# Kernel tuning notes

Hardware: AMD Instinct MI355X
Metric: run time of the kernel (lower is better)

Reference implementation:

```python
import jax, jax.numpy as jnp
import numpy as np

B, H, W, C = 4, 64, 64, 32
M1 = M2 = 16
N = H * W          # 4096 grid nodes per sample
E = 131072         # edges (avg degree 32)
EDIM = 6           # edge feature dim
KMID = 64          # kernel MLP hidden width
EPS = 1e-5         # InstanceNorm eps


def _gelu(x):
    return jax.nn.gelu(x, approximate=False)  # torch nn.GELU default is exact erf


def _mlp(x, w1, b1, w2, b2):
    return _gelu(x @ w1 + b1) @ w2 + b2


def _inorm(x):
    # torch InstanceNorm2d(affine=False) applied to [B,H,W,C]: normalizes over last two dims
    m = x.mean(axis=(2, 3), keepdims=True)
    v = x.var(axis=(2, 3), keepdims=True)
    return (x - m) * jax.lax.rsqrt(v + EPS)


def _lin_init(k, fin, fout):
    lim = 1.0 / np.sqrt(fin)
    kw, kb = jax.random.split(k)
    w = jax.random.uniform(kw, (fin, fout), jnp.float32, -lim, lim)
    b = jax.random.uniform(kb, (fout,), jnp.float32, -lim, lim)
    return w, b


def setup_inputs() -> dict:
    key = jax.random.key(0)
    ks = jax.random.split(key, 14)
    s = 1.0 / (C * C)
    inp = {}
    inp['nodes'] = jax.random.normal(ks[0], (B, H, W, C), jnp.float32)
    inp['edge_index'] = jax.random.randint(ks[1], (2, E), 0, N, dtype=jnp.int64)
    inp['edge_attr'] = jax.random.uniform(ks[2], (E, EDIM), jnp.float32)
    # spectral conv complex weights, stored as real/imag float32 pairs
    inp['w1_re'] = s * jax.random.uniform(ks[3], (C, C, M1, M2), jnp.float32)
    inp['w1_im'] = s * jax.random.uniform(ks[4], (C, C, M1, M2), jnp.float32)
    inp['w2_re'] = s * jax.random.uniform(ks[5], (C, C, M1, M2), jnp.float32)
    inp['w2_im'] = s * jax.random.uniform(ks[6], (C, C, M1, M2), jnp.float32)
    # self.mlp : MLP(C, C, 2C)
    inp['mlp_w1'], inp['mlp_b1'] = _lin_init(ks[7], C, 2 * C)
    inp['mlp_w2'], inp['mlp_b2'] = _lin_init(ks[8], 2 * C, C)
    # self.w : MLP(C, C, 2C)
    inp['wm_w1'], inp['wm_b1'] = _lin_init(ks[9], C, 2 * C)
    inp['wm_w2'], inp['wm_b2'] = _lin_init(ks[10], 2 * C, C)
    # GNO kernel MLP : EDIM -> KMID -> C*C
    inp['ker_w1'], inp['ker_b1'] = _lin_init(ks[11], EDIM, KMID)
    inp['ker_w2'], inp['ker_b2'] = _lin_init(ks[12], KMID, C * C)
    # NNConv root weight and bias (PyG uniform(size) init with size=in_channels)
    lim = 1.0 / np.sqrt(C)
    kr, kb = jax.random.split(ks[13])
    inp['root'] = jax.random.uniform(kr, (C, C), jnp.float32, -lim, lim)
    inp['gbias'] = jax.random.uniform(kb, (C,), jnp.float32, -lim, lim)
    return inp


def reference(nodes, edge_index, edge_attr, w1_re, w1_im, w2_re, w2_im,
              mlp_w1, mlp_b1, mlp_w2, mlp_b2, wm_w1, wm_b1, wm_w2, wm_b2,
              ker_w1, ker_b1, ker_w2, ker_b2, root, gbias):
    x = _inorm(nodes)                                             # [B,H,W,C]

    # --- spectral conv branch ---
    x_ft = jnp.fft.rfftn(x, axes=(1, 2), norm='ortho')            # [B,H,W//2+1,C]
    w1 = (w1_re + 1j * w1_im).astype(jnp.complex64)
    w2 = (w2_re + 1j * w2_im).astype(jnp.complex64)
    top = jnp.einsum('bxyi,ioxy->bxyo', x_ft[:, :M1, :M2, :], w1)
    bot = jnp.einsum('bxyi,ioxy->bxyo', x_ft[:, -M1:, :M2, :], w2)
    out_ft = jnp.zeros((B, H, W // 2 + 1, C), jnp.complex64)
    out_ft = out_ft.at[:, :M1, :M2, :].set(top).at[:, -M1:, :M2, :].set(bot)
    x1 = jnp.fft.irfftn(out_ft, axes=(1, 2), s=(H, W), norm='ortho')
    x1 = _mlp(_inorm(x1), mlp_w1, mlp_b1, mlp_w2, mlp_b2)         # [B,H,W,C]

    # --- pointwise MLP branch ---
    x2 = _inorm(_mlp(x, wm_w1, wm_b1, wm_w2, wm_b2))              # [B,H,W,C]

    # --- edge-conditioned GNO branch ---
    x3 = x.reshape(B, N, C)
    wmat = _mlp(edge_attr, ker_w1, ker_b1, ker_w2, ker_b2).reshape(E, C, C)
    src, dst = edge_index[0], edge_index[1]
    msg = jnp.einsum('bec,eco->beo', x3[:, src, :], wmat)         # [B,E,C]
    agg = jnp.zeros((B, N, C), jnp.float32).at[:, dst, :].add(msg)
    x3 = agg + x3 @ root + gbias                                  # [B,N,C]

    return _gelu(x1 + x2 + x3.reshape(B, H, W, C))
```

## Files before the change

### kernel.cpp

```cpp
#include <hip/hip_runtime.h>

#define B_ 4
#define H_ 64
#define W_ 64
#define C_ 32
#define N_ 4096
#define E_ 131072

typedef _Float16 half8 __attribute__((ext_vector_type(8)));
typedef float f32x4 __attribute__((ext_vector_type(4)));

__device__ __forceinline__ float gelu_f(float x) {
    return 0.5f * x * (1.0f + erff(x * 0.70710678118654752f));
}

#define TWOPI_64 (6.2831853071795864769f / 64.0f)

__device__ __forceinline__ void block_reduce2(float& s, float& s2, float* red) {
    #pragma unroll
    for (int off = 32; off > 0; off >>= 1) {
        s  += __shfl_down(s, off, 64);
        s2 += __shfl_down(s2, off, 64);
    }
    int lane = threadIdx.x & 63, wv = threadIdx.x >> 6;
    __syncthreads();
    if (lane == 0) { red[wv] = s; red[wv + 4] = s2; }
    __syncthreads();
    s  = red[0] + red[1] + red[2] + red[3];
    s2 = red[4] + red[5] + red[6] + red[7];
}

__global__ __launch_bounds__(256, 4) void k_pre(const float* __restrict__ nodes,
                                                const float* __restrict__ w2,
                                                float* __restrict__ xn,
                                                float* __restrict__ agg,
                                                float* __restrict__ Gre, float* __restrict__ Gim,
                                                _Float16* __restrict__ whi, _Float16* __restrict__ wlo) {
    int t = threadIdx.x;
    if (blockIdx.x >= 256) {
        int g0 = (blockIdx.x - 256) * 512 + t;
        #pragma unroll 1
        for (int rep = 0; rep < 2; ++rep) {
            int g = g0 + rep * 256;
            int j = g & 7, l = (g >> 3) & 63, fid = g >> 9;
            int i = fid >> 2, t2 = (fid >> 1) & 1, kh = fid & 1;
            int quad = l >> 4, l15 = l & 15;
            int k = kh * 32 + quad * 8 + j;
            int n = i * 32 + t2 * 16 + l15;
            float v = w2[k * 1024 + n];
            _Float16 hi = (_Float16)v;
            whi[g] = hi;
            wlo[g] = (_Float16)(v - (float)hi);
        }
        return;
    }
    int bh = blockIdx.x;
    __shared__ float sx[2048];
    __shared__ float tc[64], ts[64];
    __shared__ float red[8];
    const float4* src = (const float4*)(nodes + bh * 2048);
    float4* dst = (float4*)(xn + bh * 2048);
    float4* az = (float4*)(agg + bh * 2048);
    if (t < 64) { float a = TWOPI_64 * t; tc[t] = cosf(a); ts[t] = sinf(a); }
    float4 v0 = src[t * 2], v1 = src[t * 2 + 1];
    float s  = v0.x + v0.y + v0.z + v0.w + v1.x + v1.y + v1.z + v1.w;
    float s2 = v0.x*v0.x + v0.y*v0.y + v0.z*v0.z + v0.w*v0.w
             + v1.x*v1.x + v1.y*v1.y + v1.z*v1.z + v1.w*v1.w;
    block_reduce2(s, s2, red);
    float mean = s * (1.0f / 2048.0f);
    float var  = s2 * (1.0f / 2048.0f) - mean * mean;
    float sc = rsqrtf(var + 1e-5f);
    v0.x = (v0.x - mean) * sc; v0.y = (v0.y - mean) * sc;
    v0.z = (v0.z - mean) * sc; v0.w = (v0.w - mean) * sc;
    v1.x = (v1.x - mean) * sc; v1.y = (v1.y - mean) * sc;
    v1.z = (v1.z - mean) * sc; v1.w = (v1.w - mean) * sc;
    dst[t * 2] = v0; dst[t * 2 + 1] = v1;
    float4 z = {0.f, 0.f, 0.f, 0.f};
    az[t * 2] = z; az[t * 2 + 1] = z;
    ((float4*)sx)[t * 2] = v0;
    ((float4*)sx)[t * 2 + 1] = v1;
    __syncthreads();
    #pragma unroll 1
    for (int rep = 0; rep < 2; ++rep) {
        int oi = rep * 256 + t;
        int ky = oi >> 5, i = oi & 31;
        float re = 0.f, im = 0.f;
        #pragma unroll 8
        for (int w = 0; w < 64; ++w) {
            float v = sx[w * 32 + i];
            int m = (ky * w) & 63;
            re += v * tc[m];
            im -= v * ts[m];
        }
        Gre[bh * 512 + oi] = re;
        Gim[bh * 512 + oi] = im;
    }
}

__global__ __launch_bounds__(256, 4) void k_gnofxy(
        const float* __restrict__ Gre, const float* __restrict__ Gim,
        const float* __restrict__ w1re, const float* __restrict__ w1im,
        const float* __restrict__ w2re, const float* __restrict__ w2im,
        float* __restrict__ Yr, float* __restrict__ Yi,
        const float* __restrict__ ea,
        const float* __restrict__ kw1, const float* __restrict__ kb1,
        const float* __restrict__ kb2,
        const _Float16* __restrict__ whi, const _Float16* __restrict__ wlo,
        const float* __restrict__ xn,
        const int* __restrict__ ei,
        float* __restrict__ agg) {
    __shared__ __align__(16) float sbufF[4624];
    __shared__ float sB2[1024];
    __shared__ int ssrc[64], sdst[64];
    int t = threadIdx.x;

    if (blockIdx.x < 128) {
        float* tc  = sbufF;
        float* ts  = sbufF + 64;
        float* sXr = sbufF + 128;
        float* sXi = sbufF + 656;
        int bid = blockIdx.x;
        int b = bid >> 5, kxi = bid & 31;
        int kx = kxi + (kxi < 16 ? 0 : 32);
        int x = kxi & 15;
        const float* wre = (kxi < 16) ? w1re : w2re;
        const float* wim = (kxi < 16) ? w1im : w2im;
        if (t < 64) { float a = TWOPI_64 * t; tc[t] = cosf(a); ts[t] = sinf(a); }
        __syncthreads();
        #pragma unroll 1
        for (int rep = 0; rep < 2; ++rep) {
            int oi = rep * 256 + t;
            int ky = oi >> 5, i = oi & 31;
            float re = 0.f, im = 0.f;
            #pragma unroll 8
            for (int h = 0; h < 64; ++h) {
                int gidx = (b * 64 + h) * 512 + ky * 32 + i;
                float gr = Gre[gidx], gi = Gim[gidx];
                int m = (kx * h) & 63;
                float c = tc[m], sv = ts[m];
                re += gr * c + gi * sv;
                im += gi * c - gr * sv;
            }
            sXr[ky * 33 + i] = re;
            sXi[ky * 33 + i] = im;
        }
        __syncthreads();
        #pragma unroll 1
        for (int rep = 0; rep < 2; ++rep) {
            int oi = rep * 256 + t;
            int ky = oi & 15, o = oi >> 4;
            float re = 0.f, im = 0.f;
            #pragma unroll 4
            for (int i = 0; i < 32; ++i) {
                float xr = sXr[ky * 33 + i], xi = sXi[ky * 33 + i];
                int widx = (i * 32 + o) * 256 + x * 16 + ky;
                float wr = wre[widx], wi = wim[widx];
                re += xr * wr - xi * wi;
                im += xr * wi + xi * wr;
            }
            Yr[bid * 512 + ky * 32 + o] = re;
            Yi[bid * 512 + ky * 32 + o] = im;
        }
        return;
    }

    _Float16* sxTh = (_Float16*)sbufF;
    int lane = t & 63, wv = t >> 6, quad = lane >> 4, l15 = lane & 15;
    int eg = wv >> 1;
    int t2 = wv & 1;
    int e0 = (blockIdx.x - 128) * 64;

    if (t < 64) ssrc[t] = ei[e0 + t];
    else if (t < 128) sdst[t - 64] = ei[E_ + e0 + t - 64];
    for (int f = t; f < 1024; f += 256) sB2[f] = kb2[f];
    {
        int r = t >> 2, k0 = (t & 3) * 16;
        const float* ep = ea + (e0 + r) * 6;
        float e6[6];
        #pragma unroll
        for (int d = 0; d < 6; ++d) e6[d] = ep[d];
        #pragma unroll
        for (int kk = 0; kk < 16; ++kk) {
            int k = k0 + kk;
            float acc = kb1[k];
            #pragma unroll
            for (int d = 0; d < 6; ++d) acc += e6[d] * kw1[d * 64 + k];
            sbufF[r * 68 + k] = gelu_f(acc);
        }
    }
    __syncthreads();

    half8 ahi[2][2], alo[2][2];
    #pragma unroll
    for (int et = 0; et < 2; ++et) {
        #pragma unroll
        for (int kh = 0; kh < 2; ++kh) {
            const float* hp = sbufF + (eg * 32 + et * 16 + l15) * 68 + kh * 32 + quad * 8;
            float4 h0 = *(const float4*)hp;
            float4 h1 = *(const float4*)(hp + 4);
            float hv[8] = {h0.x, h0.y, h0.z, h0.w, h1.x, h1.y, h1.z, h1.w};
            half8 hh, hl;
            #pragma unroll
            for (int j = 0; j < 8; ++j) {
                _Float16 hi = (_Float16)hv[j];
                hh[j] = hi;
                hl[j] = (_Float16)(hv[j] - (float)hi);
            }
            ahi[et][kh] = hh;
            alo[et][kh] = hl;
        }
    }
    __syncthreads();

    {
        int b = t & 3, r = t >> 2;
        int s = ssrc[r];
        int pe = (r >> 5) * 32 + ((r >> 2) & 3) * 8 + ((r >> 4) & 1) * 4 + (r & 3);
        const float4* xp = (const float4*)(xn + (b * 4096 + s) * 32);
        _Float16* dp = sxTh + b * 2312 + pe;
        #pragma unroll
        for (int q = 0; q < 8; ++q) {
            float4 v = xp[q];
            dp[(q * 4 + 0) * 72] = (_Float16)v.x;
            dp[(q * 4 + 1) * 72] = (_Float16)v.y;
            dp[(q * 4 + 2) * 72] = (_Float16)v.z;
            dp[(q * 4 + 3) * 72] = (_Float16)v.w;
        }
    }
    __syncthreads();

    float msg[4][2][4];
    #pragma unroll
    for (int b = 0; b < 4; ++b)
        #pragma unroll
        for (int et = 0; et < 2; ++et)
            #pragma unroll
            for (int r = 0; r < 4; ++r) msg[b][et][r] = 0.f;

    for (int i = 0; i < 32; ++i) {
        float b2v = sB2[i * 32 + t2 * 16 + l15];
        int f0 = (i * 4 + t2 * 2) * 512 + lane * 8;
        half8 bhi0 = *(const half8*)(whi + f0);
        half8 bhi1 = *(const half8*)(whi + f0 + 512);
        half8 blo0 = *(const half8*)(wlo + f0);
        half8 blo1 = *(const half8*)(wlo + f0 + 512);
        f32x4 acc[2];
        #pragma unroll
        for (int et = 0; et < 2; ++et) {
            f32x4 a = {b2v, b2v, b2v, b2v};
            a = __builtin_amdgcn_mfma_f32_16x16x32_f16(ahi[et][0], bhi0, a, 0, 0, 0);
            a = __builtin_amdgcn_mfma_f32_16x16x32_f16(ahi[et][1], bhi1, a, 0, 0, 0);
            a = __builtin_amdgcn_mfma_f32_16x16x32_f16(ahi[et][0], blo0, a, 0, 0, 0);
            a = __builtin_amdgcn_mfma_f32_16x16x32_f16(ahi[et][1], blo1, a, 0, 0, 0);
            a = __builtin_amdgcn_mfma_f32_16x16x32_f16(alo[et][0], bhi0, a, 0, 0, 0);
            a = __builtin_amdgcn_mfma_f32_16x16x32_f16(alo[et][1], bhi1, a, 0, 0, 0);
            acc[et] = a;
        }
        #pragma unroll
        for (int b = 0; b < 4; ++b) {
            const half8 xv = *(const half8*)(sxTh + b * 2312 + i * 72 + eg * 32 + quad * 8);
            #pragma unroll
            for (int et = 0; et < 2; ++et) {
                msg[b][et][0] += (float)xv[et * 4 + 0] * acc[et][0];
                msg[b][et][1] += (float)xv[et * 4 + 1] * acc[et][1];
                msg[b][et][2] += (float)xv[et * 4 + 2] * acc[et][2];
                msg[b][et][3] += (float)xv[et * 4 + 3] * acc[et][3];
            }
        }
    }

    int o = t2 * 16 + l15;
    #pragma unroll
    for (int et = 0; et < 2; ++et) {
        #pragma unroll
        for (int r = 0; r < 4; ++r) {
            int row = eg * 32 + et * 16 + quad * 4 + r;
            int d = sdst[row];
            #pragma unroll
            for (int b = 0; b < 4; ++b) {
                atomicAdd(&agg[(b * 4096 + d) * 32 + o], msg[b][et][r]);
            }
        }
    }
}

__global__ __launch_bounds__(256, 4) void k_zx12(const float* __restrict__ Yr, const float* __restrict__ Yi,
                                                 const float* __restrict__ mw1, const float* __restrict__ mb1,
                                                 const float* __restrict__ mw2, const float* __restrict__ mb2,
                                                 const float* __restrict__ ww1, const float* __restrict__ wb1,
                                                 const float* __restrict__ ww2, const float* __restrict__ wb2,
                                                 const float* __restrict__ xn,
                                                 float* __restrict__ osum) {
    int bh = blockIdx.x;
    int b = bh >> 6, h = bh & 63;
    int t = threadIdx.x;
    __shared__ float tc[64], ts[64];
    __shared__ float red[8];
    __shared__ float sZr[528], sZi[528];
    __shared__ float sP[2112];
    __shared__ float sH[4160];
    __shared__ float sW1[2048], sW2[2048];
    __shared__ float sX[2112];
    if (t < 64) { float a = TWOPI_64 * t; tc[t] = cosf(a); ts[t] = sinf(a); }
    for (int f = t; f < 2048; f += 256) { sW1[f] = mw1[f]; sW2[f] = mw2[f]; }
    __syncthreads();
    #pragma unroll 1
    for (int rep = 0; rep < 2; ++rep) {
        int oi = rep * 256 + t;
        int ky = oi >> 5, o = oi & 31;
        float re = 0.f, im = 0.f;
        #pragma unroll 4
        for (int kxi = 0; kxi < 32; ++kxi) {
            int kx = kxi + (kxi < 16 ? 0 : 32);
            int m = (kx * h) & 63;
            float c = tc[m], sv = ts[m];
            int yidx = (b * 32 + kxi) * 512 + ky * 32 + o;
            float yr = Yr[yidx], yi = Yi[yidx];
            re += yr * c - yi * sv;
            im += yr * sv + yi * c;
        }
        sZr[ky * 33 + o] = re;
        sZi[ky * 33 + o] = im;
    }
    __syncthreads();
    float s = 0.f, s2 = 0.f;
    #pragma unroll 1
    for (int rep = 0; rep < 8; ++rep) {
        int idx = rep * 256 + t;
        int w = idx >> 5, o = idx & 31;
        float acc = sZr[o];
        #pragma unroll
        for (int ky = 1; ky < 16; ++ky) {
            int m = (ky * w) & 63;
            acc += 2.0f * (sZr[ky * 33 + o] * tc[m] - sZi[ky * 33 + o] * ts[m]);
        }
        acc *= (1.0f / 4096.0f);
        sP[w * 33 + o] = acc;
        s += acc; s2 += acc * acc;
    }
    block_reduce2(s, s2, red);
    float mean = s * (1.0f / 2048.0f);
    float sc = rsqrtf(s2 * (1.0f / 2048.0f) - mean * mean + 1e-5f);
    #pragma unroll 1
    for (int rep = 0; rep < 8; ++rep) {
        int idx = rep * 256 + t;
        int w = idx >> 5, o = idx & 31;
        sP[w * 33 + o] = (sP[w * 33 + o] - mean) * sc;
    }
    __syncthreads();
    #pragma unroll 1
    for (int rep = 0; rep < 16; ++rep) {
        int idx = rep * 256 + t;
        int w = idx >> 6, k = idx & 63;
        float acc = mb1[k];
        #pragma unroll 4
        for (int c = 0; c < 32; ++c) acc += sP[w * 33 + c] * sW1[c * 64 + k];
        sH[w * 65 + k] = gelu_f(acc);
    }
    __syncthreads();
    #pragma unroll 1
    for (int rep = 0; rep < 8; ++rep) {
        int idx = rep * 256 + t;
        int w = idx >> 5, o = idx & 31;
        float acc = mb2[o];
        #pragma unroll 4
        for (int k = 0; k < 64; ++k) acc += sH[w * 65 + k] * sW2[k * 32 + o];
        sP[w * 33 + o] = acc;
        sX[w * 33 + o] = xn[bh * 2048 + idx];
    }
    __syncthreads();
    for (int f = t; f < 2048; f += 256) { sW1[f] = ww1[f]; sW2[f] = ww2[f]; }
    __syncthreads();
    #pragma unroll 1
    for (int rep = 0; rep < 16; ++rep) {
        int idx = rep * 256 + t;
        int w = idx >> 6, k = idx & 63;
        float acc = wb1[k];
        #pragma unroll 4
        for (int c = 0; c < 32; ++c) acc += sX[w * 33 + c] * sW1[c * 64 + k];
        sH[w * 65 + k] = gelu_f(acc);
    }
    __syncthreads();
    s = 0.f; s2 = 0.f;
    #pragma unroll 1
    for (int rep = 0; rep < 8; ++rep) {
        int idx = rep * 256 + t;
        int w = idx >> 5, o = idx & 31;
        float acc = wb2[o];
        #pragma unroll 4
        for (int k = 0; k < 64; ++k) acc += sH[w * 65 + k] * sW2[k * 32 + o];
        sX[w * 33 + o] = acc;
        s += acc; s2 += acc * acc;
    }
    block_reduce2(s, s2, red);
    mean = s * (1.0f / 2048.0f);
    sc = rsqrtf(s2 * (1.0f / 2048.0f) - mean * mean + 1e-5f);
    #pragma unroll 1
    for (int rep = 0; rep < 8; ++rep) {
        int idx = rep * 256 + t;
        int w = idx >> 5, o = idx & 31;
        osum[bh * 2048 + idx] = sP[w * 33 + o] + (sX[w * 33 + o] - mean) * sc;
    }
}

__global__ __launch_bounds__(256, 4) void k_final(const float* __restrict__ osum, const float* __restrict__ agg,
                                                  const float* __restrict__ xn, const float* __restrict__ root,
                                                  const float* __restrict__ gbias, float* __restrict__ out) {
    int bh = blockIdx.x;
    int t = threadIdx.x;
    __shared__ float sX[64 * 33];
    __shared__ float sR[1024];
    for (int f = t; f < 2048; f += 256) sX[(f >> 5) * 33 + (f & 31)] = xn[bh * 2048 + f];
    for (int f = t; f < 1024; f += 256) sR[f] = root[f];
    __syncthreads();
    #pragma unroll 1
    for (int rep = 0; rep < 8; ++rep) {
        int idx = rep * 256 + t;
        int w = idx >> 5, o = idx & 31;
        float acc = gbias[o] + osum[bh * 2048 + idx] + agg[bh * 2048 + idx];
        #pragma unroll 4
        for (int c = 0; c < 32; ++c) acc += sX[w * 33 + c] * sR[c * 32 + o];
        out[bh * 2048 + idx] = gelu_f(acc);
    }
}

extern "C" void kernel_launch(void* const* d_in, const int* in_sizes, int n_in,
                              void* d_out, int out_size, void* d_ws, size_t ws_size,
                              hipStream_t stream) {
    (void)in_sizes; (void)n_in; (void)out_size; (void)ws_size;
    const float* nodes  = (const float*)d_in[0];
    const int*   eidx   = (const int*)d_in[1];
    const float* eattr  = (const float*)d_in[2];
    const float* w1re   = (const float*)d_in[3];
    const float* w1im   = (const float*)d_in[4];
    const float* w2re   = (const float*)d_in[5];
    const float* w2im   = (const float*)d_in[6];
    const float* mlp_w1 = (const float*)d_in[7];
    const float* mlp_b1 = (const float*)d_in[8];
    const float* mlp_w2 = (const float*)d_in[9];
    const float* mlp_b2 = (const float*)d_in[10];
    const float* wm_w1  = (const float*)d_in[11];
    const float* wm_b1  = (const float*)d_in[12];
    const float* wm_w2  = (const float*)d_in[13];
    const float* wm_b2  = (const float*)d_in[14];
    const float* ker_w1 = (const float*)d_in[15];
    const float* ker_b1 = (const float*)d_in[16];
    const float* ker_w2 = (const float*)d_in[17];
    const float* ker_b2 = (const float*)d_in[18];
    const float* root   = (const float*)d_in[19];
    const float* gbias  = (const float*)d_in[20];
    float* out = (float*)d_out;

    char* ws = (char*)d_ws;
    size_t off = 0;
    auto alloc = [&](size_t bytes) {
        void* p = ws + off;
        off += (bytes + 255) & ~(size_t)255;
        return p;
    };
    float* xn   = (float*)alloc(524288 * 4);
    float* agg  = (float*)alloc(524288 * 4);
    float* osum = (float*)alloc(524288 * 4);
    float* Gre  = (float*)alloc(131072 * 4);
    float* Gim  = (float*)alloc(131072 * 4);
    float* Yr   = (float*)alloc(65536 * 4);
    float* Yi   = (float*)alloc(65536 * 4);
    _Float16* whi = (_Float16*)alloc(65536 * 2);
    _Float16* wlo = (_Float16*)alloc(65536 * 2);

    k_pre<<<384, 256, 0, stream>>>(nodes, ker_w2, xn, agg, Gre, Gim, whi, wlo);
    k_gnofxy<<<2176, 256, 0, stream>>>(Gre, Gim, w1re, w1im, w2re, w2im, Yr, Yi,
                                       eattr, ker_w1, ker_b1, ker_b2, whi, wlo, xn, eidx, agg);
    k_zx12<<<256, 256, 0, stream>>>(Yr, Yi, mlp_w1, mlp_b1, mlp_w2, mlp_b2,
                                    wm_w1, wm_b1, wm_w2, wm_b2, xn, osum);
    k_final<<<256, 256, 0, stream>>>(osum, agg, xn, root, gbias, out);
}
```

Baseline: 254.0 us.

## Split GNO edge blocks across two kernels to overlap spectral stages

Factors the edge-message GNO work into a shared device function and splits its 2048 edge blocks: 1408 run alongside the forward spectral contraction in k_g1, and the remaining 640 run alongside the inverse DFT plus the spectral MLP in k_g2. The pointwise MLP branch with its InstanceNorm moves into the final kernel, which also fuses the root matmul and GELU. The aim is to fill idle compute units during the small spectral stages with independent GNO work. The cost is larger shared-memory footprints, which may lower occupancy, and a heavier final kernel running at lower launch-bounds occupancy.

```diff
diff --git a/kernel.cpp b/kernel.cpp
--- a/kernel.cpp
+++ b/kernel.cpp
@@ -1,10 +1,5 @@
 #include <hip/hip_runtime.h>
 
-#define B_ 4
-#define H_ 64
-#define W_ 64
-#define C_ 32
-#define N_ 4096
 #define E_ 131072
 
 typedef _Float16 half8 __attribute__((ext_vector_type(8)));
@@ -28,6 +23,128 @@
     __syncthreads();
     s  = red[0] + red[1] + red[2] + red[3];
     s2 = red[4] + red[5] + red[6] + red[7];
+}
+
+__device__ __forceinline__ void gno_body(int e0, float* sbufF, float* sB2, int* ssrc, int* sdst,
+                                         const float* __restrict__ ea,
+                                         const float* __restrict__ kw1, const float* __restrict__ kb1,
+                                         const float* __restrict__ kb2,
+                                         const _Float16* __restrict__ whi, const _Float16* __restrict__ wlo,
+                                         const float* __restrict__ xn, const int* __restrict__ ei,
+                                         float* __restrict__ agg) {
+    _Float16* sxTh = (_Float16*)sbufF;
+    int t = threadIdx.x;
+    int lane = t & 63, wv = t >> 6, quad = lane >> 4, l15 = lane & 15;
+    int eg = wv >> 1, t2 = wv & 1;
+
+    if (t < 64) ssrc[t] = ei[e0 + t];
+    else if (t < 128) sdst[t - 64] = ei[E_ + e0 + t - 64];
+    for (int f = t; f < 1024; f += 256) sB2[f] = kb2[f];
+    {
+        int r = t >> 2, k0 = (t & 3) * 16;
+        const float* ep = ea + (e0 + r) * 6;
+        float e6[6];
+        #pragma unroll
+        for (int d = 0; d < 6; ++d) e6[d] = ep[d];
+        #pragma unroll
+        for (int kk = 0; kk < 16; ++kk) {
+            int k = k0 + kk;
+            float acc = kb1[k];
+            #pragma unroll
+            for (int d = 0; d < 6; ++d) acc += e6[d] * kw1[d * 64 + k];
+            sbufF[r * 68 + k] = gelu_f(acc);
+        }
+    }
+    __syncthreads();
+    half8 ahi[2][2], alo[2][2];
+    #pragma unroll
+    for (int et = 0; et < 2; ++et) {
+        #pragma unroll
+        for (int kh = 0; kh < 2; ++kh) {
+            const float* hp = sbufF + (eg * 32 + et * 16 + l15) * 68 + kh * 32 + quad * 8;
+            float4 h0 = *(const float4*)hp;
+            float4 h1 = *(const float4*)(hp + 4);
+            float hv[8] = {h0.x, h0.y, h0.z, h0.w, h1.x, h1.y, h1.z, h1.w};
+            half8 hh, hl;
+            #pragma unroll
+            for (int j = 0; j < 8; ++j) {
+                _Float16 hi = (_Float16)hv[j];
+                hh[j] = hi;
+                hl[j] = (_Float16)(hv[j] - (float)hi);
+            }
+            ahi[et][kh] = hh;
+            alo[et][kh] = hl;
+        }
+    }
+    __syncthreads();
+    {
+        int b = t & 3, r = t >> 2;
+        int s = ssrc[r];
+        int pe = (r >> 5) * 32 + ((r >> 2) & 3) * 8 + ((r >> 4) & 1) * 4 + (r & 3);
+        const float4* xp = (const float4*)(xn + (b * 4096 + s) * 32);
+        _Float16* dp = sxTh + b * 2312 + pe;
+        #pragma unroll
+        for (int q = 0; q < 8; ++q) {
+            float4 v = xp[q];
+            dp[(q * 4 + 0) * 72] = (_Float16)v.x;
+            dp[(q * 4 + 1) * 72] = (_Float16)v.y;
+            dp[(q * 4 + 2) * 72] = (_Float16)v.z;
+            dp[(q * 4 + 3) * 72] = (_Float16)v.w;
+        }
+    }
+    __syncthreads();
+    float msg[4][2][4];
+    #pragma unroll
+    for (int b = 0; b < 4; ++b)
+        #pragma unroll
+        for (int et = 0; et < 2; ++et)
+            #pragma unroll
+            for (int r = 0; r < 4; ++r) msg[b][et][r] = 0.f;
+
+    for (int i = 0; i < 32; ++i) {
+        float b2v = sB2[i * 32 + t2 * 16 + l15];
+        int f0 = (i * 4 + t2 * 2) * 512 + lane * 8;
+        half8 bhi0 = *(const half8*)(whi + f0);
+        half8 bhi1 = *(const half8*)(whi + f0 + 512);
+        half8 blo0 = *(const half8*)(wlo + f0);
+        half8 blo1 = *(const half8*)(wlo + f0 + 512);
+        f32x4 acc[2];
+        #pragma unroll
+        for (int et = 0; et < 2; ++et) {
+            f32x4 ac = {b2v, b2v, b2v, b2v};
+            ac = __builtin_amdgcn_mfma_f32_16x16x32_f16(ahi[et][0], bhi0, ac, 0, 0, 0);
+            ac = __builtin_amdgcn_mfma_f32_16x16x32_f16(ahi[et][1], bhi1, ac, 0, 0, 0);
+            ac = __builtin_amdgcn_mfma_f32_16x16x32_f16(ahi[et][0], blo0, ac, 0, 0, 0);
+            ac = __builtin_amdgcn_mfma_f32_16x16x32_f16(ahi[et][1], blo1, ac, 0, 0, 0);
+            ac = __builtin_amdgcn_mfma_f32_16x16x32_f16(alo[et][0], bhi0, ac, 0, 0, 0);
+            ac = __builtin_amdgcn_mfma_f32_16x16x32_f16(alo[et][1], bhi1, ac, 0, 0, 0);
+            acc[et] = ac;
+        }
+        #pragma unroll
+        for (int b = 0; b < 4; ++b) {
+            const half8 xv = *(const half8*)(sxTh + b * 2312 + i * 72 + eg * 32 + quad * 8);
+            #pragma unroll
+            for (int et = 0; et < 2; ++et) {
+                msg[b][et][0] += (float)xv[et * 4 + 0] * acc[et][0];
+                msg[b][et][1] += (float)xv[et * 4 + 1] * acc[et][1];
+                msg[b][et][2] += (float)xv[et * 4 + 2] * acc[et][2];
+                msg[b][et][3] += (float)xv[et * 4 + 3] * acc[et][3];
+            }
+        }
+    }
+    int o = t2 * 16 + l15;
+    #pragma unroll
+    for (int et = 0; et < 2; ++et) {
+        #pragma unroll
+        for (int r = 0; r < 4; ++r) {
+            int row = eg * 32 + et * 16 + quad * 4 + r;
+            int d = sdst[row];
+            #pragma unroll
+            for (int b = 0; b < 4; ++b) {
+                atomicAdd(&agg[(b * 4096 + d) * 32 + o], msg[b][et][r]);
+            }
+        }
+    }
 }
 
 __global__ __launch_bounds__(256, 4) void k_pre(const float* __restrict__ nodes,
@@ -97,7 +214,7 @@
     }
 }
 
-__global__ __launch_bounds__(256, 4) void k_gnofxy(
+__global__ __launch_bounds__(256, 4) void k_g1(
         const float* __restrict__ Gre, const float* __restrict__ Gim,
         const float* __restrict__ w1re, const float* __restrict__ w1im,
         const float* __restrict__ w2re, const float* __restrict__ w2im,
@@ -109,16 +226,15 @@
         const float* __restrict__ xn,
         const int* __restrict__ ei,
         float* __restrict__ agg) {
-    __shared__ __align__(16) float sbufF[4624];
-    __shared__ float sB2[1024];
+    __shared__ __align__(16) float U[5648];
     __shared__ int ssrc[64], sdst[64];
     int t = threadIdx.x;
 
     if (blockIdx.x < 128) {
-        float* tc  = sbufF;
-        float* ts  = sbufF + 64;
-        float* sXr = sbufF + 128;
-        float* sXi = sbufF + 656;
+        float* tc  = U;
+        float* ts  = U + 64;
+        float* sXr = U + 128;
+        float* sXi = U + 656;
         int bid = blockIdx.x;
         int b = bid >> 5, kxi = bid & 31;
         int kx = kxi + (kxi < 16 ? 0 : 32);
@@ -163,213 +279,129 @@
         }
         return;
     }
-
-    _Float16* sxTh = (_Float16*)sbufF;
-    int lane = t & 63, wv = t >> 6, quad = lane >> 4, l15 = lane & 15;
-    int eg = wv >> 1;
-    int t2 = wv & 1;
-    int e0 = (blockIdx.x - 128) * 64;
-
-    if (t < 64) ssrc[t] = ei[e0 + t];
-    else if (t < 128) sdst[t - 64] = ei[E_ + e0 + t - 64];
-    for (int f = t; f < 1024; f += 256) sB2[f] = kb2[f];
-    {
-        int r = t >> 2, k0 = (t & 3) * 16;
-        const float* ep = ea + (e0 + r) * 6;
-        float e6[6];
-        #pragma unroll
-        for (int d = 0; d < 6; ++d) e6[d] = ep[d];
-        #pragma unroll
-        for (int kk = 0; kk < 16; ++kk) {
-            int k = k0 + kk;
-            float acc = kb1[k];
-            #pragma unroll
-            for (int d = 0; d < 6; ++d) acc += e6[d] * kw1[d * 64 + k];
-            sbufF[r * 68 + k] = gelu_f(acc);
-        }
-    }
-    __syncthreads();
-
-    half8 ahi[2][2], alo[2][2];
-    #pragma unroll
-    for (int et = 0; et < 2; ++et) {
-        #pragma unroll
-        for (int kh = 0; kh < 2; ++kh) {
-            const float* hp = sbufF + (eg * 32 + et * 16 + l15) * 68 + kh * 32 + quad * 8;
-            float4 h0 = *(const float4*)hp;
-            float4 h1 = *(const float4*)(hp + 4);
-            float hv[8] = {h0.x, h0.y, h0.z, h0.w, h1.x, h1.y, h1.z, h1.w};
-            half8 hh, hl;
-            #pragma unroll
-            for (int j = 0; j < 8; ++j) {
-                _Float16 hi = (_Float16)hv[j];
-                hh[j] = hi;
-                hl[j] = (_Float16)(hv[j] - (float)hi);
-            }
-            ahi[et][kh] = hh;
-            alo[et][kh] = hl;
-        }
-    }
-    __syncthreads();
-
-    {
-        int b = t & 3, r = t >> 2;
-        int s = ssrc[r];
-        int pe = (r >> 5) * 32 + ((r >> 2) & 3) * 8 + ((r >> 4) & 1) * 4 + (r & 3);
-        const float4* xp = (const float4*)(xn + (b * 4096 + s) * 32);
-        _Float16* dp = sxTh + b * 2312 + pe;
-        #pragma unroll
-        for (int q = 0; q < 8; ++q) {
-            float4 v = xp[q];
-            dp[(q * 4 + 0) * 72] = (_Float16)v.x;
-            dp[(q * 4 + 1) * 72] = (_Float16)v.y;
-            dp[(q * 4 + 2) * 72] = (_Float16)v.z;
-            dp[(q * 4 + 3) * 72] = (_Float16)v.w;
-        }
-    }
-    __syncthreads();
-
-    float msg[4][2][4];
-    #pragma unroll
-    for (int b = 0; b < 4; ++b)
-        #pragma unroll
-        for (int et = 0; et < 2; ++et)
-            #pragma unroll
-            for (int r = 0; r < 4; ++r) msg[b][et][r] = 0.f;
-
-    for (int i = 0; i < 32; ++i) {
-        float b2v = sB2[i * 32 + t2 * 16 + l15];
-        int f0 = (i * 4 + t2 * 2) * 512 + lane * 8;
-        half8 bhi0 = *(const half8*)(whi + f0);
-        half8 bhi1 = *(const half8*)(whi + f0 + 512);
-        half8 blo0 = *(const half8*)(wlo + f0);
-        half8 blo1 = *(const half8*)(wlo + f0 + 512);
-        f32x4 acc[2];
-        #pragma unroll
-        for (int et = 0; et < 2; ++et) {
-            f32x4 a = {b2v, b2v, b2v, b2v};
-            a = __builtin_amdgcn_mfma_f32_16x16x32_f16(ahi[et][0], bhi0, a, 0, 0, 0);
-            a = __builtin_amdgcn_mfma_f32_16x16x32_f16(ahi[et][1], bhi1, a, 0, 0, 0);
-            a = __builtin_amdgcn_mfma_f32_16x16x32_f16(ahi[et][0], blo0, a, 0, 0, 0);
-            a = __builtin_amdgcn_mfma_f32_16x16x32_f16(ahi[et][1], blo1, a, 0, 0, 0);
-            a = __builtin_amdgcn_mfma_f32_16x16x32_f16(alo[et][0], bhi0, a, 0, 0, 0);
-            a = __builtin_amdgcn_mfma_f32_16x16x32_f16(alo[et][1], bhi1, a, 0, 0, 0);
-            acc[et] = a;
-        }
-        #pragma unroll
-        for (int b = 0; b < 4; ++b) {
-            const half8 xv = *(const half8*)(sxTh + b * 2312 + i * 72 + eg * 32 + quad * 8);
-            #pragma unroll
-            for (int et = 0; et < 2; ++et) {
-                msg[b][et][0] += (float)xv[et * 4 + 0] * acc[et][0];
-                msg[b][et][1] += (float)xv[et * 4 + 1] * acc[et][1];
-                msg[b][et][2] += (float)xv[et * 4 + 2] * acc[et][2];
-                msg[b][et][3] += (float)xv[et * 4 + 3] * acc[et][3];
-            }
-        }
-    }
-
-    int o = t2 * 16 + l15;
-    #pragma unroll
-    for (int et = 0; et < 2; ++et) {
-        #pragma unroll
-        for (int r = 0; r < 4; ++r) {
-            int row = eg * 32 + et * 16 + quad * 4 + r;
-            int d = sdst[row];
-            #pragma unroll
-            for (int b = 0; b < 4; ++b) {
-                atomicAdd(&agg[(b * 4096 + d) * 32 + o], msg[b][et][r]);
-            }
-        }
-    }
-}
-
-__global__ __launch_bounds__(256, 4) void k_zx12(const float* __restrict__ Yr, const float* __restrict__ Yi,
-                                                 const float* __restrict__ mw1, const float* __restrict__ mb1,
-                                                 const float* __restrict__ mw2, const float* __restrict__ mb2,
-                                                 const float* __restrict__ ww1, const float* __restrict__ wb1,
-                                                 const float* __restrict__ ww2, const float* __restrict__ wb2,
-                                                 const float* __restrict__ xn,
-                                                 float* __restrict__ osum) {
+    gno_body((blockIdx.x - 128) * 64, U, U + 4624, ssrc, sdst,
+             ea, kw1, kb1, kb2, whi, wlo, xn, ei, agg);
+}
+
+__global__ __launch_bounds__(256, 4) void k_g2(
+        const float* __restrict__ Yr, const float* __restrict__ Yi,
+        const float* __restrict__ mw1, const float* __restrict__ mb1,
+        const float* __restrict__ mw2, const float* __restrict__ mb2,
+        float* __restrict__ osum,
+        const float* __restrict__ ea,
+        const float* __restrict__ kw1, const float* __restrict__ kb1,
+        const float* __restrict__ kb2,
+        const _Float16* __restrict__ whi, const _Float16* __restrict__ wlo,
+        const float* __restrict__ xn,
+        const int* __restrict__ ei,
+        float* __restrict__ agg) {
+    __shared__ __align__(16) float U[11584];
+    __shared__ int ssrc[64], sdst[64];
+    int t = threadIdx.x;
+
+    if (blockIdx.x < 256) {
+        int bh = blockIdx.x;
+        int b = bh >> 6, h = bh & 63;
+        float* tc  = U;
+        float* ts  = U + 64;
+        float* red = U + 128;
+        float* sZr = U + 136;
+        float* sZi = U + 664;
+        float* sP  = U + 1192;
+        float* sW1 = U + 3304;
+        float* sW2 = U + 5352;
+        float* sH  = U + 7400;
+        if (t < 64) { float a = TWOPI_64 * t; tc[t] = cosf(a); ts[t] = sinf(a); }
+        for (int f = t; f < 2048; f += 256) { sW1[f] = mw1[f]; sW2[f] = mw2[f]; }
+        __syncthreads();
+        #pragma unroll 1
+        for (int rep = 0; rep < 2; ++rep) {
+            int oi = rep * 256 + t;
+            int ky = oi >> 5, o = oi & 31;
+            float re = 0.f, im = 0.f;
+            #pragma unroll 4
+            for (int kxi = 0; kxi < 32; ++kxi) {
+                int kx = kxi + (kxi < 16 ? 0 : 32);
+                int m = (kx * h) & 63;
+                float c = tc[m], sv = ts[m];
+                int yidx = (b * 32 + kxi) * 512 + ky * 32 + o;
+                float yr = Yr[yidx], yi = Yi[yidx];
+                re += yr * c - yi * sv;
+                im += yr * sv + yi * c;
+            }
+            sZr[ky * 33 + o] = re;
+            sZi[ky * 33 + o] = im;
+        }
+        __syncthreads();
+        float s = 0.f, s2 = 0.f;
+        #pragma unroll 1
+        for (int rep = 0; rep < 8; ++rep) {
+            int idx = rep * 256 + t;
+            int w = idx >> 5, o = idx & 31;
+            float acc = sZr[o];
+            #pragma unroll
+            for (int ky = 1; ky < 16; ++ky) {
+                int m = (ky * w) & 63;
+                acc += 2.0f * (sZr[ky * 33 + o] * tc[m] - sZi[ky * 33 + o] * ts[m]);
+            }
+            acc *= (1.0f / 4096.0f);
+            sP[w * 33 + o] = acc;
+            s += acc; s2 += acc * acc;
+        }
+        block_reduce2(s, s2, red);
+        float mean = s * (1.0f / 2048.0f);
+        float sc = rsqrtf(s2 * (1.0f / 2048.0f) - mean * mean + 1e-5f);
+        #pragma unroll 1
+        for (int rep = 0; rep < 8; ++rep) {
+            int idx = rep * 256 + t;
+            int w = idx >> 5, o = idx & 31;
+            sP[w * 33 + o] = (sP[w * 33 + o] - mean) * sc;
+        }
+        __syncthreads();
+        #pragma unroll 1
+        for (int rep = 0; rep < 16; ++rep) {
+            int idx = rep * 256 + t;
+            int w = idx >> 6, k = idx & 63;
+            float acc = mb1[k];
+            #pragma unroll 4
+            for (int c = 0; c < 32; ++c) acc += sP[w * 33 + c] * sW1[c * 64 + k];
+            sH[w * 65 + k] = gelu_f(acc);
+        }
+        __syncthreads();
+        #pragma unroll 1
+        for (int rep = 0; rep < 8; ++rep) {
+            int idx = rep * 256 + t;
+            int w = idx >> 5, o = idx & 31;
+            float acc = mb2[o];
+            #pragma unroll 4
+            for (int k = 0; k < 64; ++k) acc += sH[w * 65 + k] * sW2[k * 32 + o];
+            osum[bh * 2048 + idx] = acc;
+        }
+        return;
+    }
+    gno_body((1408 + blockIdx.x - 256) * 64, U, U + 4624, ssrc, sdst,
+             ea, kw1, kb1, kb2, whi, wlo, xn, ei, agg);
+}
+
+__global__ __launch_bounds__(256, 2) void k_final2(const float* __restrict__ osum, const float* __restrict__ agg,
+                                                   const float* __restrict__ xn,
+                                                   const float* __restrict__ ww1, const float* __restrict__ wb1,
+                                                   const float* __restrict__ ww2, const float* __restrict__ wb2,
+                                                   const float* __restrict__ root, const float* __restrict__ gbias,
+                                                   float* __restrict__ out) {
     int bh = blockIdx.x;
-    int b = bh >> 6, h = bh & 63;
     int t = threadIdx.x;
-    __shared__ float tc[64], ts[64];
     __shared__ float red[8];
-    __shared__ float sZr[528], sZi[528];
-    __shared__ float sP[2112];
+    __shared__ float sX[2112];
     __shared__ float sH[4160];
     __shared__ float sW1[2048], sW2[2048];
-    __shared__ float sX[2112];
-    if (t < 64) { float a = TWOPI_64 * t; tc[t] = cosf(a); ts[t] = sinf(a); }
-    for (int f = t; f < 2048; f += 256) { sW1[f] = mw1[f]; sW2[f] = mw2[f]; }
-    __syncthreads();
-    #pragma unroll 1
-    for (int rep = 0; rep < 2; ++rep) {
-        int oi = rep * 256 + t;
-        int ky = oi >> 5, o = oi & 31;
-        float re = 0.f, im = 0.f;
-        #pragma unroll 4
-        for (int kxi = 0; kxi < 32; ++kxi) {
-            int kx = kxi + (kxi < 16 ? 0 : 32);
-            int m = (kx * h) & 63;
-            float c = tc[m], sv = ts[m];
-            int yidx = (b * 32 + kxi) * 512 + ky * 32 + o;
-            float yr = Yr[yidx], yi = Yi[yidx];
-            re += yr * c - yi * sv;
-            im += yr * sv + yi * c;
-        }
-        sZr[ky * 33 + o] = re;
-        sZi[ky * 33 + o] = im;
-    }
-    __syncthreads();
-    float s = 0.f, s2 = 0.f;
-    #pragma unroll 1
-    for (int rep = 0; rep < 8; ++rep) {
-        int idx = rep * 256 + t;
-        int w = idx >> 5, o = idx & 31;
-        float acc = sZr[o];
-        #pragma unroll
-        for (int ky = 1; ky < 16; ++ky) {
-            int m = (ky * w) & 63;
-            acc += 2.0f * (sZr[ky * 33 + o] * tc[m] - sZi[ky * 33 + o] * ts[m]);
-        }
-        acc *= (1.0f / 4096.0f);
-        sP[w * 33 + o] = acc;
-        s += acc; s2 += acc * acc;
-    }
-    block_reduce2(s, s2, red);
-    float mean = s * (1.0f / 2048.0f);
-    float sc = rsqrtf(s2 * (1.0f / 2048.0f) - mean * mean + 1e-5f);
-    #pragma unroll 1
-    for (int rep = 0; rep < 8; ++rep) {
-        int idx = rep * 256 + t;
-        int w = idx >> 5, o = idx & 31;
-        sP[w * 33 + o] = (sP[w * 33 + o] - mean) * sc;
-    }
-    __syncthreads();
-    #pragma unroll 1
-    for (int rep = 0; rep < 16; ++rep) {
-        int idx = rep * 256 + t;
-        int w = idx >> 6, k = idx & 63;
-        float acc = mb1[k];
-        #pragma unroll 4
-        for (int c = 0; c < 32; ++c) acc += sP[w * 33 + c] * sW1[c * 64 + k];
-        sH[w * 65 + k] = gelu_f(acc);
-    }
-    __syncthreads();
-    #pragma unroll 1
-    for (int rep = 0; rep < 8; ++rep) {
-        int idx = rep * 256 + t;
-        int w = idx >> 5, o = idx & 31;
-        float acc = mb2[o];
-        #pragma unroll 4
-        for (int k = 0; k < 64; ++k) acc += sH[w * 65 + k] * sW2[k * 32 + o];
-        sP[w * 33 + o] = acc;
-        sX[w * 33 + o] = xn[bh * 2048 + idx];
-    }
-    __syncthreads();
-    for (int f = t; f < 2048; f += 256) { sW1[f] = ww1[f]; sW2[f] = ww2[f]; }
+    __shared__ float sR[1024];
+    __shared__ float sP[2112];
+    for (int f = t; f < 2048; f += 256) {
+        sW1[f] = ww1[f]; sW2[f] = ww2[f];
+        sX[(f >> 5) * 33 + (f & 31)] = xn[bh * 2048 + f];
+    }
+    for (int f = t; f < 1024; f += 256) sR[f] = root[f];
     __syncthreads();
     #pragma unroll 1
     for (int rep = 0; rep < 16; ++rep) {
@@ -381,7 +413,7 @@
         sH[w * 65 + k] = gelu_f(acc);
     }
     __syncthreads();
-    s = 0.f; s2 = 0.f;
+    float s = 0.f, s2 = 0.f;
     #pragma unroll 1
     for (int rep = 0; rep < 8; ++rep) {
         int idx = rep * 256 + t;
@@ -389,35 +421,18 @@
         float acc = wb2[o];
         #pragma unroll 4
         for (int k = 0; k < 64; ++k) acc += sH[w * 65 + k] * sW2[k * 32 + o];
-        sX[w * 33 + o] = acc;
+        sP[w * 33 + o] = acc;
         s += acc; s2 += acc * acc;
     }
     block_reduce2(s, s2, red);
-    mean = s * (1.0f / 2048.0f);
-    sc = rsqrtf(s2 * (1.0f / 2048.0f) - mean * mean + 1e-5f);
+    float mean = s * (1.0f / 2048.0f);
+    float sc = rsqrtf(s2 * (1.0f / 2048.0f) - mean * mean + 1e-5f);
     #pragma unroll 1
     for (int rep = 0; rep < 8; ++rep) {
         int idx = rep * 256 + t;
         int w = idx >> 5, o = idx & 31;
-        osum[bh * 2048 + idx] = sP[w * 33 + o] + (sX[w * 33 + o] - mean) * sc;
-    }
-}
-
-__global__ __launch_bounds__(256, 4) void k_final(const float* __restrict__ osum, const float* __restrict__ agg,
-                                                  const float* __restrict__ xn, const float* __restrict__ root,
-                                                  const float* __restrict__ gbias, float* __restrict__ out) {
-    int bh = blockIdx.x;
-    int t = threadIdx.x;
-    __shared__ float sX[64 * 33];
-    __shared__ float sR[1024];
-    for (int f = t; f < 2048; f += 256) sX[(f >> 5) * 33 + (f & 31)] = xn[bh * 2048 + f];
-    for (int f = t; f < 1024; f += 256) sR[f] = root[f];
-    __syncthreads();
-    #pragma unroll 1
-    for (int rep = 0; rep < 8; ++rep) {
-        int idx = rep * 256 + t;
-        int w = idx >> 5, o = idx & 31;
-        float acc = gbias[o] + osum[bh * 2048 + idx] + agg[bh * 2048 + idx];
+        float acc = gbias[o] + osum[bh * 2048 + idx] + agg[bh * 2048 + idx]
+                  + (sP[w * 33 + o] - mean) * sc;
         #pragma unroll 4
         for (int c = 0; c < 32; ++c) acc += sX[w * 33 + c] * sR[c * 32 + o];
         out[bh * 2048 + idx] = gelu_f(acc);
@@ -469,9 +484,9 @@
     _Float16* wlo = (_Float16*)alloc(65536 * 2);
 
     k_pre<<<384, 256, 0, stream>>>(nodes, ker_w2, xn, agg, Gre, Gim, whi, wlo);
-    k_gnofxy<<<2176, 256, 0, stream>>>(Gre, Gim, w1re, w1im, w2re, w2im, Yr, Yi,
-                                       eattr, ker_w1, ker_b1, ker_b2, whi, wlo, xn, eidx, agg);
-    k_zx12<<<256, 256, 0, stream>>>(Yr, Yi, mlp_w1, mlp_b1, mlp_w2, mlp_b2,
-                                    wm_w1, wm_b1, wm_w2, wm_b2, xn, osum);
-    k_final<<<256, 256, 0, stream>>>(osum, agg, xn, root, gbias, out);
-}
+    k_g1<<<1536, 256, 0, stream>>>(Gre, Gim, w1re, w1im, w2re, w2im, Yr, Yi,
+                                   eattr, ker_w1, ker_b1, ker_b2, whi, wlo, xn, eidx, agg);
+    k_g2<<<896, 256, 0, stream>>>(Yr, Yi, mlp_w1, mlp_b1, mlp_w2, mlp_b2, osum,
+                                  eattr, ker_w1, ker_b1, ker_b2, whi, wlo, xn, eidx, agg);
+    k_final2<<<256, 256, 0, stream>>>(osum, agg, xn, wm_w1, wm_b1, wm_w2, wm_b2, root, gbias, out);
+}
```

New measurement: 256.2 us. Within noise of the previous version (+0.8%).
